# Optimization experiments

Hardware: AMD Instinct MI355X
Metric: run time of the kernel (lower is better)

The kernel has to match this reference:

```python
import jax, jax.numpy as jnp
import numpy as np
import math

B, S, D, H, NF = 2, 2048, 1024, 16, 4
DH = D // H


def setup_inputs() -> dict:
    key = jax.random.key(0)
    ks = jax.random.split(key, 8)
    scale = 0.01 / math.sqrt(D)  # rough attenuated-kaiming scale for projections
    return {
        "x": jax.random.normal(ks[0], (B, S, D), dtype=jnp.float32),
        "weights": jax.random.uniform(ks[1], (1, NF), dtype=jnp.float32),
        "Wq": jax.random.normal(ks[2], (D, D), dtype=jnp.float32) * scale,
        "bq": jnp.zeros((D,), dtype=jnp.float32),
        "Wk": jax.random.normal(ks[3], (D, D), dtype=jnp.float32) * scale,
        "bk": jnp.zeros((D,), dtype=jnp.float32),
        "Wv": jax.random.normal(ks[4], (D, D), dtype=jnp.float32) * scale,
        "bv": jnp.zeros((D,), dtype=jnp.float32),
        "Wout": jax.random.normal(ks[5], (NF, D, D), dtype=jnp.float32) / math.sqrt(D),
        "bout": jnp.zeros((NF, D), dtype=jnp.float32),
    }


def reference(x, weights, Wq, bq, Wk, bk, Wv, bv, Wout, bout):
    # projections (torch Linear: x @ W.T + b)
    q = x @ Wq.T + bq  # [B,S,D]
    k = x @ Wk.T + bk
    v = x @ Wv.T + bv
    # split heads -> [B,H,S,DH]
    split = lambda t: t.reshape(B, S, H, DH).transpose(0, 2, 1, 3)
    q, k, v = split(q), split(k), split(v)
    # scores with causal additive mask of -10000 (as in get_attention_mask)
    scores = jnp.einsum("bhqd,bhkd->bhqk", q, k) / math.sqrt(DH)
    i = jnp.arange(S)
    causal = (i[None, :] <= i[:, None])  # [S,S] True where allowed
    mask = (1.0 - causal.astype(scores.dtype)) * -10000.0
    attn = jax.nn.softmax(scores + mask, axis=-1)
    # dropout is disabled (p=0.0)
    out = jnp.einsum("bhqk,bhkd->bhqd", attn, v)  # [B,H,S,DH]
    out = out.transpose(0, 2, 1, 3).reshape(B, S, D)
    # WeightedFunctions: per-function Linear(d,d) combined by weights[0]
    w0 = weights[0]  # [NF]
    Weff = jnp.einsum("f,fod->od", w0, Wout)  # [D,D]
    beff = w0 @ bout  # [D]
    return out @ Weff.T + beff
```

## Files before the change

### kernel.cpp

```cpp
#include <hip/hip_runtime.h>


typedef unsigned short u16;
typedef __bf16 bf16_t;
typedef bf16_t bf16x8 __attribute__((ext_vector_type(8)));
typedef bf16_t bf16x4 __attribute__((ext_vector_type(4)));
typedef float f32x4 __attribute__((ext_vector_type(4)));
typedef u16 u16x8 __attribute__((ext_vector_type(8)));
typedef u16 u16x4 __attribute__((ext_vector_type(4)));

#define DEV __device__ __forceinline__

DEV u16 f2bf(float f) {
  unsigned u = __float_as_uint(f);
  u += 0x7FFFu + ((u >> 16) & 1u);
  return (u16)(u >> 16);
}

DEV void async_ld16(const void* g, void* lds_wave_uniform) {
  __builtin_amdgcn_global_load_lds(
      (const __attribute__((address_space(1))) void*)g,
      (__attribute__((address_space(3))) void*)lds_wave_uniform, 16, 0, 0);
}

__global__ __launch_bounds__(256) void prep_kernel(
    const float* __restrict__ x, const float* __restrict__ Wq,
    const float* __restrict__ Wk, const float* __restrict__ Wv,
    const float* __restrict__ w4, const float* __restrict__ Wout,
    const float* __restrict__ bout, u16* __restrict__ xbf,
    u16* __restrict__ wqkv, u16* __restrict__ Weff, float* __restrict__ beff) {
  constexpr int NX = 1048576;
  constexpr int NW = 262144;
  const int stride = gridDim.x * 256;
  for (int id = blockIdx.x * 256 + threadIdx.x; id < NX + 3 * NW + NW;
       id += stride) {
    if (id < NX) {
      const float4 v = ((const float4*)x)[id];
      u16x4 o;
      o[0] = f2bf(v.x); o[1] = f2bf(v.y); o[2] = f2bf(v.z); o[3] = f2bf(v.w);
      ((u16x4*)xbf)[id] = o;
    } else if (id < NX + 3 * NW) {
      const int wi = id - NX;
      const int which = wi >> 18, j = wi & (NW - 1);
      const float* src = which == 0 ? Wq : (which == 1 ? Wk : Wv);
      const float4 v = ((const float4*)src)[j];
      u16x4 o;
      o[0] = f2bf(v.x); o[1] = f2bf(v.y); o[2] = f2bf(v.z); o[3] = f2bf(v.w);
      ((u16x4*)wqkv)[wi] = o;
    } else {
      const int i = id - NX - 3 * NW;
      const float w0 = w4[0], w1 = w4[1], w2 = w4[2], w3 = w4[3];
      const float4* W = (const float4*)Wout;
      const float4 a = W[i], b1 = W[NW + i], b2 = W[2 * NW + i],
                   b3 = W[3 * NW + i];
      u16x4 o;
      o[0] = f2bf(w0 * a.x + w1 * b1.x + w2 * b2.x + w3 * b3.x);
      o[1] = f2bf(w0 * a.y + w1 * b1.y + w2 * b2.y + w3 * b3.y);
      o[2] = f2bf(w0 * a.z + w1 * b1.z + w2 * b2.z + w3 * b3.z);
      o[3] = f2bf(w0 * a.w + w1 * b1.w + w2 * b2.w + w3 * b3.w);
      ((u16x4*)Weff)[i] = o;
      if (i < 256) {
        const float4* B4 = (const float4*)bout;
        const float4 ba = B4[i], c1 = B4[256 + i], c2 = B4[512 + i],
                     c3 = B4[768 + i];
        float4 ob;
        ob.x = w0 * ba.x + w1 * c1.x + w2 * c2.x + w3 * c3.x;
        ob.y = w0 * ba.y + w1 * c1.y + w2 * c2.y + w3 * c3.y;
        ob.z = w0 * ba.z + w1 * c1.z + w2 * c2.z + w3 * c3.z;
        ob.w = w0 * ba.w + w1 * c1.w + w2 * c2.w + w3 * c3.w;
        ((float4*)beff)[i] = ob;
      }
    }
  }
}


__global__ __launch_bounds__(256) void gemm_bt_kernel(
    const u16* __restrict__ A, const u16* __restrict__ Bw,
    const float* __restrict__ bias, float* __restrict__ C, int M, int N, int K) {
  __shared__ u16 LDS[32768];
  const int tid = threadIdx.x;
  const int w = tid >> 6, lane = tid & 63;
  const int l15 = lane & 15, l4 = lane >> 4;
  const int wr = w >> 1, wc = w & 1;
  const long m0 = (long)blockIdx.y * 128, n0 = (long)blockIdx.x * 128;

  int srow[4], scol[4];
#pragma unroll
  for (int d = 0; d < 4; ++d) {
    srow[d] = d * 32 + w * 8 + (lane >> 3);
    scol[d] = ((lane & 7) ^ (srow[d] & 7)) * 8;
  }
  auto stage = [&](int buf, int kt) {
#pragma unroll
    for (int d = 0; d < 4; ++d) {
      async_ld16(A + (m0 + srow[d]) * K + kt + scol[d],
                 &LDS[buf * 8192 + d * 2048 + w * 512]);
      async_ld16(Bw + (n0 + srow[d]) * K + kt + scol[d],
                 &LDS[16384 + buf * 8192 + d * 2048 + w * 512]);
    }
  };

  f32x4 acc[4][4] = {};
  stage(0, 0);
  __syncthreads();
  const int nt = K / 64;
  for (int t = 0; t < nt; ++t) {
    const int buf = t & 1;
    if (t + 1 < nt) stage(buf ^ 1, (t + 1) * 64);
    bf16x8 af[4][2], bf[4][2];
#pragma unroll
    for (int i = 0; i < 4; ++i) {
      const int ra = wr * 64 + i * 16 + l15;
      const int rb = wc * 64 + i * 16 + l15;
#pragma unroll
      for (int ks = 0; ks < 2; ++ks) {
        af[i][ks] = *(const bf16x8*)&LDS[buf * 8192 + ra * 64 +
                                         (((ks * 4 + l4) ^ (ra & 7)) * 8)];
        bf[i][ks] = *(const bf16x8*)&LDS[16384 + buf * 8192 + rb * 64 +
                                         (((ks * 4 + l4) ^ (rb & 7)) * 8)];
      }
    }
#pragma unroll
    for (int i = 0; i < 4; ++i)
#pragma unroll
      for (int j = 0; j < 4; ++j) {
        acc[i][j] = __builtin_amdgcn_mfma_f32_16x16x32_bf16(af[i][0], bf[j][0],
                                                            acc[i][j], 0, 0, 0);
        acc[i][j] = __builtin_amdgcn_mfma_f32_16x16x32_bf16(af[i][1], bf[j][1],
                                                            acc[i][j], 0, 0, 0);
      }
    __syncthreads();
  }

#pragma unroll
  for (int i = 0; i < 4; ++i) {
    const long row0 = m0 + wr * 64 + i * 16 + l4 * 4;
#pragma unroll
    for (int j = 0; j < 4; ++j) {
      const long col = n0 + wc * 64 + j * 16 + l15;
      const float bb = bias[col];
#pragma unroll
      for (int r = 0; r < 4; ++r)
        C[(row0 + r) * N + col] = acc[i][j][r] + bb;
    }
  }
}

__global__ __launch_bounds__(256) void gemm_qkv_kernel(
    const u16* __restrict__ A, const u16* __restrict__ Bw,
    const float* __restrict__ bq, const float* __restrict__ bk,
    const float* __restrict__ bv, u16* __restrict__ qo, u16* __restrict__ ko,
    u16* __restrict__ vt) {
  constexpr int K = 1024;
  __shared__ u16 LDS[32768];
  const int tid = threadIdx.x;
  const int w = tid >> 6, lane = tid & 63;
  const int l15 = lane & 15, l4 = lane >> 4;
  const int wr = w >> 1, wc = w & 1;
  const long m0 = (long)blockIdx.y * 128, n0 = (long)blockIdx.x * 128;
  const int seg = blockIdx.x >> 3;
  const float* bias = seg == 0 ? bq : (seg == 1 ? bk : bv);
  const float scale = seg == 0 ? 0.18033688011112042f : 1.0f;

  int srow[4], scol[4];
#pragma unroll
  for (int d = 0; d < 4; ++d) {
    srow[d] = d * 32 + w * 8 + (lane >> 3);
    scol[d] = ((lane & 7) ^ (srow[d] & 7)) * 8;
  }
  auto stage = [&](int buf, int kt) {
#pragma unroll
    for (int d = 0; d < 4; ++d) {
      async_ld16(A + (m0 + srow[d]) * K + kt + scol[d],
                 &LDS[buf * 8192 + d * 2048 + w * 512]);
      async_ld16(Bw + (n0 + srow[d]) * K + kt + scol[d],
                 &LDS[16384 + buf * 8192 + d * 2048 + w * 512]);
    }
  };

  f32x4 acc[4][4] = {};
  stage(0, 0);
  __syncthreads();
  const int nt = K / 64;
  for (int t = 0; t < nt; ++t) {
    const int buf = t & 1;
    if (t + 1 < nt) stage(buf ^ 1, (t + 1) * 64);
    bf16x8 af[4][2], bf[4][2];
#pragma unroll
    for (int i = 0; i < 4; ++i) {
      const int ra = wr * 64 + i * 16 + l15;
      const int rb = wc * 64 + i * 16 + l15;
#pragma unroll
      for (int ks = 0; ks < 2; ++ks) {
        af[i][ks] = *(const bf16x8*)&LDS[buf * 8192 + ra * 64 +
                                         (((ks * 4 + l4) ^ (ra & 7)) * 8)];
        bf[i][ks] = *(const bf16x8*)&LDS[16384 + buf * 8192 + rb * 64 +
                                         (((ks * 4 + l4) ^ (rb & 7)) * 8)];
      }
    }
#pragma unroll
    for (int i = 0; i < 4; ++i)
#pragma unroll
      for (int j = 0; j < 4; ++j) {
        acc[i][j] = __builtin_amdgcn_mfma_f32_16x16x32_bf16(af[i][0], bf[j][0],
                                                            acc[i][j], 0, 0, 0);
        acc[i][j] = __builtin_amdgcn_mfma_f32_16x16x32_bf16(af[i][1], bf[j][1],
                                                            acc[i][j], 0, 0, 0);
      }
    __syncthreads();
  }

  const long ccol0 = n0 - (long)seg * 1024;
  if (seg < 2) {
    u16* outp = seg == 0 ? qo : ko;
#pragma unroll
    for (int i = 0; i < 4; ++i) {
#pragma unroll
      for (int j = 0; j < 4; ++j) {
        const int colb = wc * 64 + j * 16 + l15;
        const float bb = bias[ccol0 + colb];
#pragma unroll
        for (int r = 0; r < 4; ++r) {
          const int row = wr * 64 + i * 16 + l4 * 4 + r;
          LDS[row * 128 + (colb ^ ((row & 15) << 3))] =
              f2bf((acc[i][j][r] + bb) * scale);
        }
      }
    }
    __syncthreads();
#pragma unroll
    for (int p = 0; p < 8; ++p) {
      const int cid = p * 256 + tid;
      const int row = cid >> 4, c = cid & 15;
      const u16x8 vch = *(const u16x8*)&LDS[row * 128 + ((c ^ (row & 15)) * 8)];
      *(u16x8*)&outp[(m0 + row) * 1024 + ccol0 + c * 8] = vch;
    }
  } else {
    const int b = (int)(m0 >> 11);
    const int s0 = (int)(m0 & 2047);
#pragma unroll
    for (int i = 0; i < 4; ++i) {
#pragma unroll
      for (int j = 0; j < 4; ++j) {
        const int colb = wc * 64 + j * 16 + l15;
        const float bb = bias[ccol0 + colb];
#pragma unroll
        for (int r = 0; r < 4; ++r) {
          const int row = wr * 64 + i * 16 + l4 * 4 + r;
          LDS[colb * 128 + (row ^ ((colb & 15) << 3))] = f2bf(acc[i][j][r] + bb);
        }
      }
    }
    __syncthreads();
#pragma unroll
    for (int p = 0; p < 8; ++p) {
      const int cid = p * 256 + tid;
      const int c = cid >> 4, r0 = (cid & 15) * 8;
      const u16x8 vch = *(const u16x8*)&LDS[c * 128 + (r0 ^ ((c & 15) << 3))];
      const int gcol = (int)ccol0 + c;
      const int h = gcol >> 6, d = gcol & 63;
      *(u16x8*)&vt[(size_t)((b * 16 + h) * 64 + d) * 2048 + s0 + r0] = vch;
    }
  }
}

__global__ __launch_bounds__(512, 6) void flash_kernel(
    const u16* __restrict__ Q, const u16* __restrict__ Kg,
    const u16* __restrict__ Vt, u16* __restrict__ O,
    u16* __restrict__ accP, float* __restrict__ mP, float* __restrict__ lP) {
  constexpr int S = 2048, D = 1024, DH = 64;
  __shared__ u16 Ks[2][4096];
  __shared__ u16 Vs[2][4096];
  __shared__ u16 Ps[8192];
  const int tid = threadIdx.x;
  const int w = tid >> 6, lane = tid & 63;
  const int l15 = lane & 15, l4 = lane >> 4;
  const int bh = blockIdx.y, b = bh >> 4, h = bh & 15;
  const int x = 23 - (int)blockIdx.x;
  int bi, kvlo, kvhi, seg;
  if (x < 8) {
    bi = x; seg = -1; kvlo = 0; kvhi = 2 * bi + 2;
  } else {
    const int idx = x - 8;
    bi = 8 + (idx >> 1); seg = idx & 1;
    kvlo = seg ? (bi + 1) : 0;
    kvhi = seg ? (2 * bi + 2) : (bi + 1);
  }
  const int qw = 128 * bi + w * 16;
  const int qtile = qw >> 6;

  const u16* Kbh = Kg + (size_t)b * S * D + h * DH;
  const u16* Vbh = Vt + (size_t)bh * DH * S;

  const int srow = tid >> 3;
  const int scol = ((tid & 7) ^ (srow & 7)) * 8;
  const int sw = l15 & 7;

  bf16x8 qf[2];
  {
    const u16* qp = Q + (size_t)(b * S + qw + l15) * D + h * DH + l4 * 8;
    qf[0] = *(const bf16x8*)qp;
    qf[1] = *(const bf16x8*)(qp + 32);
  }

  f32x4 acc_o[4] = {};
  float m_run = -3e38f, l_run = 0.f;

  async_ld16(Kbh + (size_t)(kvlo * 64 + srow) * D + scol, &Ks[0][w * 512]);
  async_ld16(Vbh + (size_t)srow * S + kvlo * 64 + scol, &Vs[0][w * 512]);
  __syncthreads();

  for (int it = kvlo; it < kvhi; ++it) {
    const int buf = (it - kvlo) & 1;
    if (it + 1 < kvhi) {
      async_ld16(Kbh + (size_t)((it + 1) * 64 + srow) * D + scol,
                 &Ks[buf ^ 1][w * 512]);
      async_ld16(Vbh + (size_t)srow * S + (it + 1) * 64 + scol,
                 &Vs[buf ^ 1][w * 512]);
    }
    if (it <= qtile) {
      f32x4 accs[4] = {};
#pragma unroll
      for (int cb = 0; cb < 4; ++cb) {
        const int row = cb * 16 + l15;
        const bf16x8 kf0 = *(const bf16x8*)&Ks[buf][row * 64 + ((l4 ^ sw) * 8)];
        const bf16x8 kf1 =
            *(const bf16x8*)&Ks[buf][row * 64 + (((l4 + 4) ^ sw) * 8)];
        accs[cb] =
            __builtin_amdgcn_mfma_f32_16x16x32_bf16(kf0, qf[0], accs[cb], 0, 0, 0);
        accs[cb] =
            __builtin_amdgcn_mfma_f32_16x16x32_bf16(kf1, qf[1], accs[cb], 0, 0, 0);
      }
      float mx = -3e38f;
      if (it == qtile) {
#pragma unroll
        for (int cb = 0; cb < 4; ++cb)
#pragma unroll
          for (int r = 0; r < 4; ++r) {
            float s_ = accs[cb][r];
            if (it * 64 + cb * 16 + l4 * 4 + r > qw + l15) s_ = -3e38f;
            accs[cb][r] = s_;
            mx = fmaxf(mx, s_);
          }
      } else {
#pragma unroll
        for (int cb = 0; cb < 4; ++cb)
#pragma unroll
          for (int r = 0; r < 4; ++r) mx = fmaxf(mx, accs[cb][r]);
      }
      if (!__all(mx - m_run <= 8.0f)) {
        mx = fmaxf(mx, __shfl_xor(mx, 16));
        mx = fmaxf(mx, __shfl_xor(mx, 32));
        const float mn = fmaxf(m_run, mx);
        const float corr = __builtin_amdgcn_exp2f(m_run - mn);
        m_run = mn;
        float cq[4];
#pragma unroll
        for (int r = 0; r < 4; ++r) cq[r] = __shfl(corr, l4 * 4 + r, 64);
#pragma unroll
        for (int db = 0; db < 4; ++db)
#pragma unroll
          for (int r = 0; r < 4; ++r) acc_o[db][r] *= cq[r];
        l_run *= corr;
      }
      float rs = 0.f;
#pragma unroll
      for (int cb = 0; cb < 4; ++cb)
#pragma unroll
        for (int r = 0; r < 4; ++r) {
          const float pv = __builtin_amdgcn_exp2f(accs[cb][r] - m_run);
          accs[cb][r] = pv;
          rs += pv;
        }
      l_run += rs;
#pragma unroll
      for (int cb = 0; cb < 4; ++cb) {
        bf16x4 pk = {(bf16_t)accs[cb][0], (bf16_t)accs[cb][1],
                     (bf16_t)accs[cb][2], (bf16_t)accs[cb][3]};
        const int chunk = (2 * cb + (l4 >> 1)) ^ sw;
        *(bf16x4*)&Ps[w * 1024 + l15 * 64 + chunk * 8 + (l4 & 1) * 4] = pk;
      }
      asm volatile("s_waitcnt lgkmcnt(0)" ::: "memory");
      bf16x8 pa[2];
#pragma unroll
      for (int mf = 0; mf < 2; ++mf) {
        const int chunk = (mf * 4 + l4) ^ sw;
        pa[mf] = *(const bf16x8*)&Ps[w * 1024 + l15 * 64 + chunk * 8];
      }
#pragma unroll
      for (int db = 0; db < 4; ++db) {
        const int row = db * 16 + l15;
        const bf16x8 vf0 = *(const bf16x8*)&Vs[buf][row * 64 + ((l4 ^ sw) * 8)];
        const bf16x8 vf1 =
            *(const bf16x8*)&Vs[buf][row * 64 + (((l4 + 4) ^ sw) * 8)];
        acc_o[db] =
            __builtin_amdgcn_mfma_f32_16x16x32_bf16(pa[0], vf0, acc_o[db], 0, 0, 0);
        acc_o[db] =
            __builtin_amdgcn_mfma_f32_16x16x32_bf16(pa[1], vf1, acc_o[db], 0, 0, 0);
      }
    }
    __syncthreads();
  }

  float l_tot = l_run;
  l_tot += __shfl_xor(l_tot, 16);
  l_tot += __shfl_xor(l_tot, 32);
  float lq[4];
  if (seg < 0) {
#pragma unroll
    for (int r = 0; r < 4; ++r) lq[r] = __shfl(l_tot, l4 * 4 + r, 64);
  }
#pragma unroll
  for (int db = 0; db < 4; ++db) {
#pragma unroll
    for (int r = 0; r < 4; ++r) {
      const int row = l4 * 4 + r;
      const int col = db * 16 + l15;
      const float v = seg < 0 ? acc_o[db][r] / lq[r] : acc_o[db][r];
      Ps[w * 1024 + row * 64 + (col ^ ((row & 7) << 3))] = f2bf(v);
    }
  }
  asm volatile("s_waitcnt lgkmcnt(0)" ::: "memory");
  if (seg < 0) {
#pragma unroll
    for (int j = 0; j < 2; ++j) {
      const int cid = j * 64 + lane;
      const int row = cid >> 3, c = cid & 7;
      const u16x8 vch =
          *(const u16x8*)&Ps[w * 1024 + row * 64 + ((c ^ (row & 7)) * 8)];
      *(u16x8*)&O[(size_t)(b * S + qw + row) * D + h * DH + c * 8] = vch;
    }
  } else {
    const size_t base = (size_t)seg * 32768 + (size_t)bh * 1024 + (qw - 1024);
#pragma unroll
    for (int j = 0; j < 2; ++j) {
      const int cid = j * 64 + lane;
      const int row = cid >> 3, c = cid & 7;
      const u16x8 vch =
          *(const u16x8*)&Ps[w * 1024 + row * 64 + ((c ^ (row & 7)) * 8)];
      *(u16x8*)&accP[(base + row) * 64 + c * 8] = vch;
    }
    if (l4 == 0) {
      mP[base + l15] = m_run;
      lP[base + l15] = l_tot;
    }
  }
}

__global__ __launch_bounds__(256) void combine_kernel(
    const u16* __restrict__ accP, const float* __restrict__ mP,
    const float* __restrict__ lP, u16* __restrict__ O) {
  const int id = blockIdx.x * 256 + threadIdx.x;
  const int row = id >> 3;
  const int c0 = (id & 7) * 8;
  const float m0 = mP[row], m1 = mP[32768 + row];
  const float l0 = lP[row], l1 = lP[32768 + row];
  const float M = fmaxf(m0, m1);
  const float e0 = __builtin_amdgcn_exp2f(m0 - M);
  const float e1 = __builtin_amdgcn_exp2f(m1 - M);
  const float inv = 1.f / (l0 * e0 + l1 * e1);
  const bf16_t* aP = (const bf16_t*)accP;
  const bf16x8 a0 = *(const bf16x8*)&aP[(size_t)row * 64 + c0];
  const bf16x8 a1 = *(const bf16x8*)&aP[(size_t)(32768 + row) * 64 + c0];
  const int bh = row >> 10, s = 1024 + (row & 1023);
  const int b = bh >> 4, h = bh & 15;
  bf16_t* out = (bf16_t*)O + (size_t)(b * 2048 + s) * 1024 + h * 64 + c0;
  bf16x8 o;
#pragma unroll
  for (int j = 0; j < 8; ++j)
    o[j] = (bf16_t)(((float)a0[j] * e0 + (float)a1[j] * e1) * inv);
  *(bf16x8*)out = o;
}

extern "C" void kernel_launch(void* const* d_in, const int* in_sizes, int n_in,
                              void* d_out, int out_size, void* d_ws, size_t ws_size,
                              hipStream_t stream) {
  (void)in_sizes; (void)n_in; (void)out_size;
  const float* x   = (const float*)d_in[0];
  const float* wts = (const float*)d_in[1];
  const float* Wq  = (const float*)d_in[2];
  const float* bq  = (const float*)d_in[3];
  const float* Wk  = (const float*)d_in[4];
  const float* bk  = (const float*)d_in[5];
  const float* Wv  = (const float*)d_in[6];
  const float* bv  = (const float*)d_in[7];
  const float* Wo  = (const float*)d_in[8];
  const float* bo  = (const float*)d_in[9];
  float* out = (float*)d_out;

  if (ws_size < 58724352) return;

  char* ws = (char*)d_ws;
  u16* xbf  = (u16*)(ws + 0);
  u16* qbf  = (u16*)(ws + 8388608);
  u16* kbf  = (u16*)(ws + 16777216);
  u16* vt   = (u16*)(ws + 33554432);
  u16* attn = (u16*)(ws + 41943040);
  u16* wqkv = (u16*)(ws + 50331648);
  u16* wob  = (u16*)(ws + 56623104);
  float* beff = (float*)(ws + 58720256);

  u16* accP = xbf;
  float* mP = (float*)(ws + 50331648);
  float* lP = mP + 65536;

  prep_kernel<<<2048, 256, 0, stream>>>(x, Wq, Wk, Wv, wts, Wo, bo,
                                        xbf, wqkv, wob, beff);
  gemm_qkv_kernel<<<dim3(24, 32), 256, 0, stream>>>(xbf, wqkv, bq, bk, bv,
                                                    qbf, kbf, vt);
  flash_kernel<<<dim3(24, 32), 512, 0, stream>>>(qbf, kbf, vt, attn,
                                                 accP, mP, lP);
  combine_kernel<<<1024, 256, 0, stream>>>(accP, mP, lP, attn);
  gemm_bt_kernel<<<dim3(8, 32), 256, 0, stream>>>(
      attn, wob, beff, out, 4096, 1024, 1024);
}
```

Baseline: 108.2 us.

## Triple-buffer GEMM K-loop with BK=32 and raise MFMA wave priority

Both projection GEMMs are rewritten to use a shared three-stage LDS ring with a K-tile of 32 instead of a double buffer of 64. Loads are issued two tiles ahead, and manual vmcnt waits plus barriers replace the trailing __syncthreads. The swizzle is changed to fit the narrower rows. s_setprio is raised around the MFMA blocks in the GEMMs and in the attention kernel so that waves doing matrix math get issue priority. The goal is to hide global-load latency and cut LDS use per block, at the cost of twice as many loop iterations and barriers.

```diff
diff --git a/kernel.cpp b/kernel.cpp
--- a/kernel.cpp
+++ b/kernel.cpp
@@ -22,6 +22,8 @@
       (const __attribute__((address_space(1))) void*)g,
       (__attribute__((address_space(3))) void*)lds_wave_uniform, 16, 0, 0);
 }
+
+DEV int KF(int r) { return (r & 3) ^ ((r >> 2) & 1); }
 
 __global__ __launch_bounds__(256) void prep_kernel(
     const float* __restrict__ x, const float* __restrict__ Wq,
@@ -75,63 +77,65 @@
 }
 
 
+#define GEMM_PIPELINE_LOOP(A_, B_, m0_, n0_, K_)                               \
+  int rA[2], oA[2], dstc[2];                                                   \
+  _Pragma("unroll") for (int j = 0; j < 2; ++j) {                              \
+    const int c = (j * 4 + w) * 64 + lane;                                     \
+    rA[j] = c >> 2;                                                            \
+    oA[j] = ((c & 3) ^ KF(rA[j])) * 8;                                         \
+    dstc[j] = (j * 4 + w) * 512;                                               \
+  }                                                                            \
+  auto stage = [&](int buf, int kt) {                                          \
+    _Pragma("unroll") for (int j = 0; j < 2; ++j) {                            \
+      async_ld16(A_ + (m0_ + rA[j]) * K_ + kt + oA[j],                         \
+                 &LDS[buf * 4096 + dstc[j]]);                                  \
+      async_ld16(B_ + (n0_ + rA[j]) * K_ + kt + oA[j],                         \
+                 &LDS[12288 + buf * 4096 + dstc[j]]);                          \
+    }                                                                          \
+  };                                                                           \
+  f32x4 acc[4][4] = {};                                                        \
+  stage(0, 0);                                                                 \
+  stage(1, 32);                                                                \
+  const int nt = K_ / 32;                                                      \
+  int cur = 0, stg = 2;                                                        \
+  for (int t = 0; t < nt; ++t) {                                               \
+    if (t == nt - 1)                                                           \
+      asm volatile("s_waitcnt vmcnt(0)\ns_barrier" ::: "memory");              \
+    else                                                                       \
+      asm volatile("s_waitcnt vmcnt(4)\ns_barrier" ::: "memory");              \
+    __builtin_amdgcn_sched_barrier(0);                                         \
+    if (t + 2 < nt) stage(stg, (t + 2) * 32);                                  \
+    bf16x8 af[4], bfr[4];                                                      \
+    _Pragma("unroll") for (int i = 0; i < 4; ++i) {                            \
+      const int ra = wr * 64 + i * 16 + l15;                                   \
+      const int rb = wc * 64 + i * 16 + l15;                                   \
+      af[i] = *(const bf16x8*)&LDS[cur * 4096 + ra * 32 + ((l4 ^ KF(ra)) * 8)];\
+      bfr[i] = *(const bf16x8*)&LDS[12288 + cur * 4096 + rb * 32 +             \
+                                    ((l4 ^ KF(rb)) * 8)];                      \
+    }                                                                          \
+    asm volatile("s_waitcnt lgkmcnt(0)" ::: "memory");                         \
+    __builtin_amdgcn_sched_barrier(0);                                         \
+    __builtin_amdgcn_s_setprio(1);                                             \
+    _Pragma("unroll") for (int i = 0; i < 4; ++i)                              \
+        _Pragma("unroll") for (int j = 0; j < 4; ++j)                          \
+            acc[i][j] = __builtin_amdgcn_mfma_f32_16x16x32_bf16(               \
+                af[i], bfr[j], acc[i][j], 0, 0, 0);                            \
+    __builtin_amdgcn_s_setprio(0);                                             \
+    cur = cur == 2 ? 0 : cur + 1;                                              \
+    stg = stg == 2 ? 0 : stg + 1;                                              \
+  }
+
 __global__ __launch_bounds__(256) void gemm_bt_kernel(
     const u16* __restrict__ A, const u16* __restrict__ Bw,
     const float* __restrict__ bias, float* __restrict__ C, int M, int N, int K) {
-  __shared__ u16 LDS[32768];
+  __shared__ u16 LDS[24576];
   const int tid = threadIdx.x;
   const int w = tid >> 6, lane = tid & 63;
   const int l15 = lane & 15, l4 = lane >> 4;
   const int wr = w >> 1, wc = w & 1;
   const long m0 = (long)blockIdx.y * 128, n0 = (long)blockIdx.x * 128;
 
-  int srow[4], scol[4];
-#pragma unroll
-  for (int d = 0; d < 4; ++d) {
-    srow[d] = d * 32 + w * 8 + (lane >> 3);
-    scol[d] = ((lane & 7) ^ (srow[d] & 7)) * 8;
-  }
-  auto stage = [&](int buf, int kt) {
-#pragma unroll
-    for (int d = 0; d < 4; ++d) {
-      async_ld16(A + (m0 + srow[d]) * K + kt + scol[d],
-                 &LDS[buf * 8192 + d * 2048 + w * 512]);
-      async_ld16(Bw + (n0 + srow[d]) * K + kt + scol[d],
-                 &LDS[16384 + buf * 8192 + d * 2048 + w * 512]);
-    }
-  };
-
-  f32x4 acc[4][4] = {};
-  stage(0, 0);
-  __syncthreads();
-  const int nt = K / 64;
-  for (int t = 0; t < nt; ++t) {
-    const int buf = t & 1;
-    if (t + 1 < nt) stage(buf ^ 1, (t + 1) * 64);
-    bf16x8 af[4][2], bf[4][2];
-#pragma unroll
-    for (int i = 0; i < 4; ++i) {
-      const int ra = wr * 64 + i * 16 + l15;
-      const int rb = wc * 64 + i * 16 + l15;
-#pragma unroll
-      for (int ks = 0; ks < 2; ++ks) {
-        af[i][ks] = *(const bf16x8*)&LDS[buf * 8192 + ra * 64 +
-                                         (((ks * 4 + l4) ^ (ra & 7)) * 8)];
-        bf[i][ks] = *(const bf16x8*)&LDS[16384 + buf * 8192 + rb * 64 +
-                                         (((ks * 4 + l4) ^ (rb & 7)) * 8)];
-      }
-    }
-#pragma unroll
-    for (int i = 0; i < 4; ++i)
-#pragma unroll
-      for (int j = 0; j < 4; ++j) {
-        acc[i][j] = __builtin_amdgcn_mfma_f32_16x16x32_bf16(af[i][0], bf[j][0],
-                                                            acc[i][j], 0, 0, 0);
-        acc[i][j] = __builtin_amdgcn_mfma_f32_16x16x32_bf16(af[i][1], bf[j][1],
-                                                            acc[i][j], 0, 0, 0);
-      }
-    __syncthreads();
-  }
+  GEMM_PIPELINE_LOOP(A, Bw, m0, n0, K)
 
 #pragma unroll
   for (int i = 0; i < 4; ++i) {
@@ -153,7 +157,7 @@
     const float* __restrict__ bv, u16* __restrict__ qo, u16* __restrict__ ko,
     u16* __restrict__ vt) {
   constexpr int K = 1024;
-  __shared__ u16 LDS[32768];
+  __shared__ u16 LDS[24576];
   const int tid = threadIdx.x;
   const int w = tid >> 6, lane = tid & 63;
   const int l15 = lane & 15, l4 = lane >> 4;
@@ -163,54 +167,9 @@
   const float* bias = seg == 0 ? bq : (seg == 1 ? bk : bv);
   const float scale = seg == 0 ? 0.18033688011112042f : 1.0f;
 
-  int srow[4], scol[4];
-#pragma unroll
-  for (int d = 0; d < 4; ++d) {
-    srow[d] = d * 32 + w * 8 + (lane >> 3);
-    scol[d] = ((lane & 7) ^ (srow[d] & 7)) * 8;
-  }
-  auto stage = [&](int buf, int kt) {
-#pragma unroll
-    for (int d = 0; d < 4; ++d) {
-      async_ld16(A + (m0 + srow[d]) * K + kt + scol[d],
-                 &LDS[buf * 8192 + d * 2048 + w * 512]);
-      async_ld16(Bw + (n0 + srow[d]) * K + kt + scol[d],
-                 &LDS[16384 + buf * 8192 + d * 2048 + w * 512]);
-    }
-  };
-
-  f32x4 acc[4][4] = {};
-  stage(0, 0);
+  GEMM_PIPELINE_LOOP(A, Bw, m0, n0, K)
+
   __syncthreads();
-  const int nt = K / 64;
-  for (int t = 0; t < nt; ++t) {
-    const int buf = t & 1;
-    if (t + 1 < nt) stage(buf ^ 1, (t + 1) * 64);
-    bf16x8 af[4][2], bf[4][2];
-#pragma unroll
-    for (int i = 0; i < 4; ++i) {
-      const int ra = wr * 64 + i * 16 + l15;
-      const int rb = wc * 64 + i * 16 + l15;
-#pragma unroll
-      for (int ks = 0; ks < 2; ++ks) {
-        af[i][ks] = *(const bf16x8*)&LDS[buf * 8192 + ra * 64 +
-                                         (((ks * 4 + l4) ^ (ra & 7)) * 8)];
-        bf[i][ks] = *(const bf16x8*)&LDS[16384 + buf * 8192 + rb * 64 +
-                                         (((ks * 4 + l4) ^ (rb & 7)) * 8)];
-      }
-    }
-#pragma unroll
-    for (int i = 0; i < 4; ++i)
-#pragma unroll
-      for (int j = 0; j < 4; ++j) {
-        acc[i][j] = __builtin_amdgcn_mfma_f32_16x16x32_bf16(af[i][0], bf[j][0],
-                                                            acc[i][j], 0, 0, 0);
-        acc[i][j] = __builtin_amdgcn_mfma_f32_16x16x32_bf16(af[i][1], bf[j][1],
-                                                            acc[i][j], 0, 0, 0);
-      }
-    __syncthreads();
-  }
-
   const long ccol0 = n0 - (long)seg * 1024;
   if (seg < 2) {
     u16* outp = seg == 0 ? qo : ko;
@@ -321,6 +280,7 @@
     }
     if (it <= qtile) {
       f32x4 accs[4] = {};
+      __builtin_amdgcn_s_setprio(1);
 #pragma unroll
       for (int cb = 0; cb < 4; ++cb) {
         const int row = cb * 16 + l15;
@@ -332,6 +292,7 @@
         accs[cb] =
             __builtin_amdgcn_mfma_f32_16x16x32_bf16(kf1, qf[1], accs[cb], 0, 0, 0);
       }
+      __builtin_amdgcn_s_setprio(0);
       float mx = -3e38f;
       if (it == qtile) {
 #pragma unroll
@@ -388,6 +349,7 @@
         const int chunk = (mf * 4 + l4) ^ sw;
         pa[mf] = *(const bf16x8*)&Ps[w * 1024 + l15 * 64 + chunk * 8];
       }
+      __builtin_amdgcn_s_setprio(1);
 #pragma unroll
       for (int db = 0; db < 4; ++db) {
         const int row = db * 16 + l15;
@@ -399,6 +361,7 @@
         acc_o[db] =
             __builtin_amdgcn_mfma_f32_16x16x32_bf16(pa[1], vf1, acc_o[db], 0, 0, 0);
       }
+      __builtin_amdgcn_s_setprio(0);
     }
     __syncthreads();
   }
```

Measured after the change: 108.8 us (median of 2 runs). No clear change (+0.5%).
